# Kernel optimization log

Measured on AMD Instinct MI355X. Metric: run time of the kernel, lower is better.

## Reference

```python
import jax, jax.numpy as jnp
import numpy as np

N, E, H, L, G, C = 50000, 800000, 64, 4, 500, 10
BN_EPS = 1e-5


def setup_inputs() -> dict:
    key = jax.random.key(0)
    ks = jax.random.split(key, 24)
    x = jax.random.normal(ks[0], (N, H), dtype=jnp.float32)
    edge_index = jax.random.randint(ks[1], (2, E), 0, N, dtype=jnp.int64)
    batch = jnp.sort(jax.random.randint(ks[2], (N,), 0, G, dtype=jnp.int64))
    s = 1.0 / np.sqrt(H)
    # stacked per-layer GIN MLP params: Linear->BN->ReLU->Linear->BN->ReLU
    conv_W1 = jax.random.uniform(ks[3], (L, H, H), minval=-s, maxval=s, dtype=jnp.float32)
    conv_b1 = jax.random.uniform(ks[4], (L, H), minval=-s, maxval=s, dtype=jnp.float32)
    bn1_g = jax.random.uniform(ks[5], (L, H), minval=0.5, maxval=1.5, dtype=jnp.float32)
    bn1_b = jax.random.normal(ks[6], (L, H), dtype=jnp.float32) * 0.1
    bn1_m = jax.random.normal(ks[7], (L, H), dtype=jnp.float32) * 0.1
    bn1_v = jax.random.uniform(ks[8], (L, H), minval=0.5, maxval=1.5, dtype=jnp.float32)
    conv_W2 = jax.random.uniform(ks[9], (L, H, H), minval=-s, maxval=s, dtype=jnp.float32)
    conv_b2 = jax.random.uniform(ks[10], (L, H), minval=-s, maxval=s, dtype=jnp.float32)
    bn2_g = jax.random.uniform(ks[11], (L, H), minval=0.5, maxval=1.5, dtype=jnp.float32)
    bn2_b = jax.random.normal(ks[12], (L, H), dtype=jnp.float32) * 0.1
    bn2_m = jax.random.normal(ks[13], (L, H), dtype=jnp.float32) * 0.1
    bn2_v = jax.random.uniform(ks[14], (L, H), minval=0.5, maxval=1.5, dtype=jnp.float32)
    s1 = 1.0 / np.sqrt(L * H)
    lin1_W = jax.random.uniform(ks[15], (L * H, H), minval=-s1, maxval=s1, dtype=jnp.float32)
    lin1_b = jax.random.uniform(ks[16], (H,), minval=-s1, maxval=s1, dtype=jnp.float32)
    lin2_W = jax.random.uniform(ks[17], (H, C), minval=-s, maxval=s, dtype=jnp.float32)
    lin2_b = jax.random.uniform(ks[18], (C,), minval=-s, maxval=s, dtype=jnp.float32)
    return dict(x=x, edge_index=edge_index, batch=batch,
                conv_W1=conv_W1, conv_b1=conv_b1, bn1_g=bn1_g, bn1_b=bn1_b, bn1_m=bn1_m, bn1_v=bn1_v,
                conv_W2=conv_W2, conv_b2=conv_b2, bn2_g=bn2_g, bn2_b=bn2_b, bn2_m=bn2_m, bn2_v=bn2_v,
                lin1_W=lin1_W, lin1_b=lin1_b, lin2_W=lin2_W, lin2_b=lin2_b)


def _bn(h, g, b, m, v):
    # eval-mode BatchNorm1d with running stats
    return g * (h - m) * jax.lax.rsqrt(v + BN_EPS) + b


def reference(x, edge_index, batch,
              conv_W1, conv_b1, bn1_g, bn1_b, bn1_m, bn1_v,
              conv_W2, conv_b2, bn2_g, bn2_b, bn2_m, bn2_v,
              lin1_W, lin1_b, lin2_W, lin2_b):
    src, dst = edge_index[0], edge_index[1]

    def layer(h, p):
        W1, b1, g1, be1, m1, v1, W2, b2, g2, be2, m2, v2 = p
        # GIN aggregation (eps=0): h_i + sum_{j->i} h_j, scatter-add over edges
        agg = jax.ops.segment_sum(h[src], dst, num_segments=N)
        z = h + agg
        z = jax.nn.relu(_bn(z @ W1 + b1, g1, be1, m1, v1))
        z = jax.nn.relu(_bn(z @ W2 + b2, g2, be2, m2, v2))
        return z, z

    params = (conv_W1, conv_b1, bn1_g, bn1_b, bn1_m, bn1_v,
              conv_W2, conv_b2, bn2_g, bn2_b, bn2_m, bn2_v)
    _, xs = jax.lax.scan(layer, x, params)          # [L, N, H]
    xcat = jnp.transpose(xs, (1, 0, 2)).reshape(N, L * H)  # JK 'cat'
    pooled = jax.ops.segment_sum(xcat, batch, num_segments=G)  # sum readout [G, L*H]
    h = jax.nn.relu(pooled @ lin1_W + lin1_b)
    # dropout is identity in eval mode
    return h @ lin2_W + lin2_b  # [G, C]
```

## Files before the change

kernel.cpp:

```cpp
#include <hip/hip_runtime.h>

#define NN 50000
#define NE 800000
#define HH 64
#define LL 4
#define GG 500
#define CC 10
#define BN_EPS 1e-5f
#define SCB 200
#define NPART 6250
#define ECHUNK 2048
#define NCHUNK 391

typedef short bf16x8 __attribute__((ext_vector_type(8)));
typedef float f32x4  __attribute__((ext_vector_type(4)));

__device__ inline float bf2f(unsigned int u16) {
    union { unsigned int i; float f; } v; v.i = u16 << 16; return v.f;
}
__device__ inline unsigned short f2bf(float f) {
    union { float f; unsigned int i; } v; v.f = f;
    unsigned int u = v.i + 0x7fffu + ((v.i >> 16) & 1u);
    return (unsigned short)(u >> 16);
}
__device__ inline void addrow8(float* acc, uint4 u) {
    #pragma unroll
    for (int q = 0; q < 4; ++q) {
        unsigned int w = (&u.x)[q];
        union { unsigned int i; float f; } lo, hi;
        lo.i = w << 16; hi.i = w & 0xffff0000u;
        acc[2 * q]     += lo.f;
        acc[2 * q + 1] += hi.f;
    }
}

__global__ __launch_bounds__(256) void k_cast(const float* __restrict__ x, unsigned short* __restrict__ xb) {
    int i = blockIdx.x * 256 + threadIdx.x;
    if (i < NN * 16) {
        float4 v = ((const float4*)x)[i];
        uint2 p;
        p.x = (unsigned int)f2bf(v.x) | ((unsigned int)f2bf(v.y) << 16);
        p.y = (unsigned int)f2bf(v.z) | ((unsigned int)f2bf(v.w) << 16);
        ((uint2*)xb)[i] = p;
    }
}

__global__ __launch_bounds__(256) void k_prepw(const float* __restrict__ cW1,
                                               const float* __restrict__ cW2,
                                               unsigned short* __restrict__ fragW)
{
    int idx = blockIdx.x * 256 + threadIdx.x;
    if (idx >= LL * 2 * 4 * 2 * 64 * 8) return;
    int j    = idx & 7;
    int lane = (idx >> 3) & 63;
    int kh   = (idx >> 9) & 1;
    int ct   = (idx >> 10) & 3;
    int g    = (idx >> 12) & 1;
    int L    = idx >> 13;
    int k = kh * 32 + (lane >> 4) * 8 + j;
    int n = ct * 16 + (lane & 15);
    const float* W = (g == 0 ? cW1 : cW2) + (size_t)L * HH * HH;
    float w = W[k * HH + n];
    unsigned short hi = f2bf(w);
    unsigned short lo = f2bf(w - bf2f(hi));
    size_t fhi = ((size_t)L * 32 + ((g * 2 + 0) * 4 + ct) * 2 + kh) * 512 + lane * 8 + j;
    size_t flo = ((size_t)L * 32 + ((g * 2 + 1) * 4 + ct) * 2 + kh) * 512 + lane * 8 + j;
    fragW[fhi] = hi;
    fragW[flo] = lo;
}

__global__ __launch_bounds__(256) void k_hist8(const int* __restrict__ dst, int* __restrict__ deg) {
    int part  = blockIdx.x & 7;
    int chunk = blockIdx.x >> 3;
    int lo = part * NPART, hi = lo + NPART;
    int base = chunk * ECHUNK + threadIdx.x;
    #pragma unroll
    for (int i = 0; i < 8; ++i) {
        int e = base + i * 256;
        if (e < NE) {
            int d = dst[e];
            if (d >= lo && d < hi) atomicAdd(&deg[d], 1);
        }
    }
}

__global__ __launch_bounds__(256) void k_scan1(const int* __restrict__ deg, int* __restrict__ incl,
                                               int* __restrict__ bsum) {
    int t = threadIdx.x;
    int idx = blockIdx.x * 256 + t;
    __shared__ int s[256];
    int v = (idx < NN) ? deg[idx] : 0;
    s[t] = v;
    __syncthreads();
    for (int off = 1; off < 256; off <<= 1) {
        int u = (t >= off) ? s[t - off] : 0;
        __syncthreads();
        if (t >= off) s[t] += u;
        __syncthreads();
    }
    if (idx < NN) incl[idx] = s[t];
    if (t == 255) bsum[blockIdx.x] = s[255];
}

__global__ __launch_bounds__(256) void k_scan2(const int* __restrict__ bsum, int* __restrict__ boff,
                                               int* __restrict__ row_ptr) {
    int t = threadIdx.x;
    __shared__ int s[256];
    int v = (t < SCB) ? bsum[t] : 0;
    s[t] = v;
    __syncthreads();
    for (int off = 1; off < 256; off <<= 1) {
        int u = (t >= off) ? s[t - off] : 0;
        __syncthreads();
        if (t >= off) s[t] += u;
        __syncthreads();
    }
    if (t < SCB) boff[t] = s[t] - v;
    if (t == 255) row_ptr[NN] = s[255];
}

__global__ __launch_bounds__(256) void k_scan3(const int* __restrict__ deg, const int* __restrict__ incl,
                                               const int* __restrict__ boff, int* __restrict__ row_ptr) {
    int idx = blockIdx.x * 256 + threadIdx.x;
    if (idx < NN) row_ptr[idx] = incl[idx] - deg[idx] + boff[blockIdx.x];
}

__global__ __launch_bounds__(256) void k_scatter8(const int* __restrict__ src, const int* __restrict__ dst,
                                                  const int* __restrict__ row_ptr, int* __restrict__ cursor,
                                                  int* __restrict__ col) {
    int part  = blockIdx.x & 7;
    int chunk = blockIdx.x >> 3;
    int lo = part * NPART, hi = lo + NPART;
    int base = chunk * ECHUNK + threadIdx.x;
    #pragma unroll
    for (int i = 0; i < 8; ++i) {
        int e = base + i * 256;
        if (e < NE) {
            int d = dst[e];
            if (d >= lo && d < hi) {
                int pos = atomicAdd(&cursor[d], 1);
                col[row_ptr[d] + pos] = src[e];
            }
        }
    }
}

__global__ __launch_bounds__(256) void k_agg(
    const unsigned short* __restrict__ hb, unsigned short* __restrict__ aggb,
    const int* __restrict__ row_ptr, const int* __restrict__ col)
{
    int tid  = threadIdx.x;
    int lane = tid & 63;
    int wave = tid >> 6;
    int gl   = lane & 7;
    int grp  = lane >> 3;
    int n = blockIdx.x * 32 + wave * 8 + grp;
    if (n >= NN) return;

    const uint4* hv = (const uint4*)hb;
    float acc[8]  = {0.f, 0.f, 0.f, 0.f, 0.f, 0.f, 0.f, 0.f};
    float acc2[8] = {0.f, 0.f, 0.f, 0.f, 0.f, 0.f, 0.f, 0.f};
    addrow8(acc, hv[(size_t)n * 8 + gl]);

    int j = row_ptr[n], fin = row_ptr[n + 1];
    for (; j + 4 <= fin; j += 4) {
        int s0 = col[j], s1 = col[j + 1], s2 = col[j + 2], s3 = col[j + 3];
        uint4 u0 = hv[(size_t)s0 * 8 + gl];
        uint4 u1 = hv[(size_t)s1 * 8 + gl];
        uint4 u2 = hv[(size_t)s2 * 8 + gl];
        uint4 u3 = hv[(size_t)s3 * 8 + gl];
        addrow8(acc, u0);  addrow8(acc2, u1);
        addrow8(acc, u2);  addrow8(acc2, u3);
    }
    for (; j < fin; ++j)
        addrow8(acc, hv[(size_t)col[j] * 8 + gl]);

    #pragma unroll
    for (int q = 0; q < 8; ++q) acc[q] += acc2[q];

    uint4 o;
    o.x = (unsigned int)f2bf(acc[0]) | ((unsigned int)f2bf(acc[1]) << 16);
    o.y = (unsigned int)f2bf(acc[2]) | ((unsigned int)f2bf(acc[3]) << 16);
    o.z = (unsigned int)f2bf(acc[4]) | ((unsigned int)f2bf(acc[5]) << 16);
    o.w = (unsigned int)f2bf(acc[6]) | ((unsigned int)f2bf(acc[7]) << 16);
    ((uint4*)(aggb + (size_t)n * HH))[gl] = o;
}

#define MT 128
#define SAB 80
#define SOF 68

__global__ __launch_bounds__(256) void k_mlp2(
    const unsigned short* __restrict__ agg, unsigned short* __restrict__ h_out,
    const int* __restrict__ batch, float* __restrict__ pooled, int layer,
    const unsigned short* __restrict__ fragW,
    const float* __restrict__ lb1, const float* __restrict__ g1,
    const float* __restrict__ bb1, const float* __restrict__ m1, const float* __restrict__ v1,
    const float* __restrict__ lb2, const float* __restrict__ g2,
    const float* __restrict__ bb2, const float* __restrict__ m2, const float* __restrict__ v2)
{
    __shared__ unsigned short sHi[128 * SAB];
    __shared__ unsigned short sLo[128 * SAB];
    __shared__ float sOut[128 * SOF];
    __shared__ float red[256];

    int tid  = threadIdx.x;
    int lane = tid & 63;
    int wave = tid >> 6;
    int l15 = lane & 15, l4 = lane >> 4;
    int base = blockIdx.x * MT;
    int wrow = wave * 32;

    float sc1v[4], sh1v[4], sc2v[4], sh2v[4];
    #pragma unroll
    for (int ct = 0; ct < 4; ++ct) {
        int c = ct * 16 + l15;
        float s1 = g1[c] * rsqrtf(v1[c] + BN_EPS);
        sc1v[ct] = s1; sh1v[ct] = (lb1[c] - m1[c]) * s1 + bb1[c];
        float s2 = g2[c] * rsqrtf(v2[c] + BN_EPS);
        sc2v[ct] = s2; sh2v[ct] = (lb2[c] - m2[c]) * s2 + bb2[c];
    }

    for (int i = tid; i < 128 * 8; i += 256) {
        int r = i >> 3, q = i & 7;
        int gr = base + r;
        uint4 u = (gr < NN) ? ((const uint4*)(agg + (size_t)gr * HH))[q] : make_uint4(0, 0, 0, 0);
        *(uint4*)&sHi[r * SAB + q * 8] = u;
    }
    __syncthreads();

    const bf16x8* fwv = (const bf16x8*)fragW + ((size_t)layer * 32) * 64;

    bf16x8 a0[2][2];
    #pragma unroll
    for (int rt = 0; rt < 2; ++rt)
        #pragma unroll
        for (int kh = 0; kh < 2; ++kh)
            a0[rt][kh] = *(const bf16x8*)&sHi[(wrow + rt * 16 + l15) * SAB + kh * 32 + l4 * 8];

    f32x4 acc[2][4];
    #pragma unroll
    for (int rt = 0; rt < 2; ++rt)
        #pragma unroll
        for (int ct = 0; ct < 4; ++ct) {
            f32x4 c = {0.f, 0.f, 0.f, 0.f};
            #pragma unroll
            for (int kh = 0; kh < 2; ++kh) {
                c = __builtin_amdgcn_mfma_f32_16x16x32_bf16(a0[rt][kh], fwv[((0 * 4 + ct) * 2 + kh) * 64 + lane], c, 0, 0, 0);
                c = __builtin_amdgcn_mfma_f32_16x16x32_bf16(a0[rt][kh], fwv[((1 * 4 + ct) * 2 + kh) * 64 + lane], c, 0, 0, 0);
            }
            acc[rt][ct] = c;
        }
    __syncthreads();

    #pragma unroll
    for (int rt = 0; rt < 2; ++rt)
        #pragma unroll
        for (int ct = 0; ct < 4; ++ct)
            #pragma unroll
            for (int rg = 0; rg < 4; ++rg) {
                int r = wrow + rt * 16 + l4 * 4 + rg;
                float z = fmaxf(fmaf(acc[rt][ct][rg], sc1v[ct], sh1v[ct]), 0.f);
                unsigned short hi = f2bf(z);
                sHi[r * SAB + ct * 16 + l15] = hi;
                sLo[r * SAB + ct * 16 + l15] = f2bf(z - bf2f(hi));
            }
    __syncthreads();

    bf16x8 ah[2][2], al[2][2];
    #pragma unroll
    for (int rt = 0; rt < 2; ++rt)
        #pragma unroll
        for (int kh = 0; kh < 2; ++kh) {
            int off = (wrow + rt * 16 + l15) * SAB + kh * 32 + l4 * 8;
            ah[rt][kh] = *(const bf16x8*)&sHi[off];
            al[rt][kh] = *(const bf16x8*)&sLo[off];
        }
    #pragma unroll
    for (int rt = 0; rt < 2; ++rt)
        #pragma unroll
        for (int ct = 0; ct < 4; ++ct) {
            f32x4 c = {0.f, 0.f, 0.f, 0.f};
            #pragma unroll
            for (int kh = 0; kh < 2; ++kh) {
                bf16x8 bh = fwv[((2 * 4 + ct) * 2 + kh) * 64 + lane];
                bf16x8 bl = fwv[((3 * 4 + ct) * 2 + kh) * 64 + lane];
                c = __builtin_amdgcn_mfma_f32_16x16x32_bf16(ah[rt][kh], bh, c, 0, 0, 0);
                c = __builtin_amdgcn_mfma_f32_16x16x32_bf16(al[rt][kh], bh, c, 0, 0, 0);
                c = __builtin_amdgcn_mfma_f32_16x16x32_bf16(ah[rt][kh], bl, c, 0, 0, 0);
            }
            #pragma unroll
            for (int rg = 0; rg < 4; ++rg) {
                int r = wrow + rt * 16 + l4 * 4 + rg;
                float z = fmaxf(fmaf(c[rg], sc2v[ct], sh2v[ct]), 0.f);
                sOut[r * SOF + ct * 16 + l15] = z;
            }
        }
    __syncthreads();

    for (int i = tid; i < 128 * 8; i += 256) {
        int r = i >> 3, q = i & 7;
        int gr = base + r;
        if (gr < NN) {
            const float* sp = &sOut[r * SOF + q * 8];
            uint4 o;
            o.x = (unsigned int)f2bf(sp[0]) | ((unsigned int)f2bf(sp[1]) << 16);
            o.y = (unsigned int)f2bf(sp[2]) | ((unsigned int)f2bf(sp[3]) << 16);
            o.z = (unsigned int)f2bf(sp[4]) | ((unsigned int)f2bf(sp[5]) << 16);
            o.w = (unsigned int)f2bf(sp[6]) | ((unsigned int)f2bf(sp[7]) << 16);
            ((uint4*)(h_out + (size_t)gr * HH))[q] = o;
        }
    }

    int thi = base + MT; if (thi > NN) thi = NN;
    int gfirst = batch[base];
    int glast  = batch[thi - 1];
    int c = tid & 63;
    int q = tid >> 6;
    for (int g = gfirst; g <= glast; ++g) {
        int lo = base, hb = thi;
        while (lo < hb) { int mid = (lo + hb) >> 1; if (batch[mid] < g) lo = mid + 1; else hb = mid; }
        int lo_g = lo;
        hb = thi;
        while (lo < hb) { int mid = (lo + hb) >> 1; if (batch[mid] < g + 1) lo = mid + 1; else hb = mid; }
        int hi_g = lo;
        float a = 0.f;
        for (int r = lo_g + q; r < hi_g; r += 4) a += sOut[(r - base) * SOF + c];
        red[tid] = a;
        __syncthreads();
        if (tid < 64)
            atomicAdd(&pooled[(size_t)g * (LL * HH) + layer * HH + c],
                      red[c] + red[64 + c] + red[128 + c] + red[192 + c]);
        __syncthreads();
    }
}

__global__ __launch_bounds__(64) void k_mlp(const float* __restrict__ pooled,
                                            const float* __restrict__ w1, const float* __restrict__ b1,
                                            const float* __restrict__ w2, const float* __restrict__ b2,
                                            float* __restrict__ out)
{
    int g = blockIdx.x, c = threadIdx.x;
    __shared__ float hh[64];
    float acc = b1[c];
    const float* p = pooled + g * (LL * HH);
    #pragma unroll 8
    for (int k = 0; k < LL * HH; ++k) acc = fmaf(p[k], w1[k * HH + c], acc);
    hh[c] = fmaxf(acc, 0.f);
    __syncthreads();
    if (c < CC) {
        float o = b2[c];
        #pragma unroll
        for (int k = 0; k < HH; ++k) o = fmaf(hh[k], w2[k * CC + c], o);
        out[g * CC + c] = o;
    }
}

extern "C" void kernel_launch(void* const* d_in, const int* in_sizes, int n_in,
                              void* d_out, int out_size, void* d_ws, size_t ws_size,
                              hipStream_t stream) {
    const float* x    = (const float*)d_in[0];
    const int*   ei   = (const int*)d_in[1];
    const int*   bat  = (const int*)d_in[2];
    const float* cW1  = (const float*)d_in[3];
    const float* cb1  = (const float*)d_in[4];
    const float* g1   = (const float*)d_in[5];
    const float* bb1  = (const float*)d_in[6];
    const float* m1   = (const float*)d_in[7];
    const float* v1   = (const float*)d_in[8];
    const float* cW2  = (const float*)d_in[9];
    const float* cb2  = (const float*)d_in[10];
    const float* g2   = (const float*)d_in[11];
    const float* bb2  = (const float*)d_in[12];
    const float* m2   = (const float*)d_in[13];
    const float* v2   = (const float*)d_in[14];
    const float* l1W  = (const float*)d_in[15];
    const float* l1b  = (const float*)d_in[16];
    const float* l2W  = (const float*)d_in[17];
    const float* l2b  = (const float*)d_in[18];

    const int* srcp = ei;
    const int* dstp = ei + NE;

    char* ws = (char*)d_ws;
    size_t off = 0;
    auto alloc = [&](size_t bytes) -> char* {
        char* p = ws + off;
        off += (bytes + 255) & ~size_t(255);
        return p;
    };
    unsigned short* xb    = (unsigned short*)alloc((size_t)NN * HH * 2);
    unsigned short* hb0   = (unsigned short*)alloc((size_t)NN * HH * 2);
    unsigned short* hb1   = (unsigned short*)alloc((size_t)NN * HH * 2);
    unsigned short* aggb  = (unsigned short*)alloc((size_t)NN * HH * 2);
    unsigned short* fragW = (unsigned short*)alloc((size_t)LL * 32 * 512 * 2);
    float* pooled  = (float*)alloc((size_t)GG * LL * HH * sizeof(float));
    int*   row_ptr = (int*)alloc((size_t)(NN + 1) * sizeof(int));
    int*   deg     = (int*)alloc((size_t)NN * sizeof(int));
    int*   incl    = (int*)alloc((size_t)NN * sizeof(int));
    int*   cursor  = (int*)alloc((size_t)NN * sizeof(int));
    int*   colx    = (int*)alloc((size_t)NE * sizeof(int));
    int*   bsum    = (int*)alloc(256 * sizeof(int));
    int*   boff    = (int*)alloc(256 * sizeof(int));

    hipMemsetAsync(deg, 0, (size_t)NN * sizeof(int), stream);
    hipMemsetAsync(cursor, 0, (size_t)NN * sizeof(int), stream);
    hipMemsetAsync(pooled, 0, (size_t)GG * LL * HH * sizeof(float), stream);

    k_hist8<<<8 * NCHUNK, 256, 0, stream>>>(dstp, deg);
    k_cast<<<NN * 16 / 256, 256, 0, stream>>>(x, xb);
    k_prepw<<<128, 256, 0, stream>>>(cW1, cW2, fragW);
    k_scan1<<<SCB, 256, 0, stream>>>(deg, incl, bsum);
    k_scan2<<<1, 256, 0, stream>>>(bsum, boff, row_ptr);
    k_scan3<<<SCB, 256, 0, stream>>>(deg, incl, boff, row_ptr);
    k_scatter8<<<8 * NCHUNK, 256, 0, stream>>>(srcp, dstp, row_ptr, cursor, colx);

    const unsigned short* hin = xb;
    unsigned short* bufs[2] = { hb0, hb1 };
    const int AGG_BLK = (NN + 31) / 32;
    const int MLP_BLK = (NN + MT - 1) / MT;
    for (int l = 0; l < LL; ++l) {
        unsigned short* hout = bufs[l & 1];
        k_agg<<<AGG_BLK, 256, 0, stream>>>(hin, aggb, row_ptr, colx);
        k_mlp2<<<MLP_BLK, 256, 0, stream>>>(aggb, hout, bat, pooled, l, fragW,
            cb1 + l * HH, g1 + l * HH, bb1 + l * HH, m1 + l * HH, v1 + l * HH,
            cb2 + l * HH, g2 + l * HH, bb2 + l * HH, m2 + l * HH, v2 + l * HH);
        hin = hout;
    }

    k_mlp<<<GG, 64, 0, stream>>>(pooled, l1W, l1b, l2W, l2b, (float*)d_out);
}
```

Before: 315.1 us.

## Merge prep kernels and scan stages, coalesce memsets, unroll aggregation by eight

Fuses the cast and weight-prep kernels into one launch, and folds the single-block scan into the final scan pass so that each block recomputes the block-offset prefix itself. The three memsets are replaced by one, made possible by placing the zeroed buffers next to each other in the workspace. The aggregation loop gains an 8-wide unrolled gather to keep more loads in flight. These reduce launch count and per-launch overhead, at the cost of redundant prefix work in every scan block and higher register pressure in k_agg.

```diff
diff --git a/kernel.cpp b/kernel.cpp
--- a/kernel.cpp
+++ b/kernel.cpp
@@ -11,6 +11,7 @@
 #define NPART 6250
 #define ECHUNK 2048
 #define NCHUNK 391
+#define CASTB 3125
 
 typedef short bf16x8 __attribute__((ext_vector_type(8)));
 typedef float f32x4  __attribute__((ext_vector_type(4)));
@@ -34,22 +35,22 @@
     }
 }
 
-__global__ __launch_bounds__(256) void k_cast(const float* __restrict__ x, unsigned short* __restrict__ xb) {
-    int i = blockIdx.x * 256 + threadIdx.x;
-    if (i < NN * 16) {
-        float4 v = ((const float4*)x)[i];
-        uint2 p;
-        p.x = (unsigned int)f2bf(v.x) | ((unsigned int)f2bf(v.y) << 16);
-        p.y = (unsigned int)f2bf(v.z) | ((unsigned int)f2bf(v.w) << 16);
-        ((uint2*)xb)[i] = p;
-    }
-}
-
-__global__ __launch_bounds__(256) void k_prepw(const float* __restrict__ cW1,
-                                               const float* __restrict__ cW2,
-                                               unsigned short* __restrict__ fragW)
+__global__ __launch_bounds__(256) void k_prep(const float* __restrict__ x, unsigned short* __restrict__ xb,
+                                              const float* __restrict__ cW1, const float* __restrict__ cW2,
+                                              unsigned short* __restrict__ fragW)
 {
-    int idx = blockIdx.x * 256 + threadIdx.x;
+    if (blockIdx.x < CASTB) {
+        int i = blockIdx.x * 256 + threadIdx.x;
+        if (i < NN * 16) {
+            float4 v = ((const float4*)x)[i];
+            uint2 p;
+            p.x = (unsigned int)f2bf(v.x) | ((unsigned int)f2bf(v.y) << 16);
+            p.y = (unsigned int)f2bf(v.z) | ((unsigned int)f2bf(v.w) << 16);
+            ((uint2*)xb)[i] = p;
+        }
+        return;
+    }
+    int idx = (blockIdx.x - CASTB) * 256 + threadIdx.x;
     if (idx >= LL * 2 * 4 * 2 * 64 * 8) return;
     int j    = idx & 7;
     int lane = (idx >> 3) & 63;
@@ -102,8 +103,8 @@
     if (t == 255) bsum[blockIdx.x] = s[255];
 }
 
-__global__ __launch_bounds__(256) void k_scan2(const int* __restrict__ bsum, int* __restrict__ boff,
-                                               int* __restrict__ row_ptr) {
+__global__ __launch_bounds__(256) void k_scan3f(const int* __restrict__ deg, const int* __restrict__ incl,
+                                                const int* __restrict__ bsum, int* __restrict__ row_ptr) {
     int t = threadIdx.x;
     __shared__ int s[256];
     int v = (t < SCB) ? bsum[t] : 0;
@@ -115,14 +116,10 @@
         if (t >= off) s[t] += u;
         __syncthreads();
     }
-    if (t < SCB) boff[t] = s[t] - v;
-    if (t == 255) row_ptr[NN] = s[255];
-}
-
-__global__ __launch_bounds__(256) void k_scan3(const int* __restrict__ deg, const int* __restrict__ incl,
-                                               const int* __restrict__ boff, int* __restrict__ row_ptr) {
-    int idx = blockIdx.x * 256 + threadIdx.x;
-    if (idx < NN) row_ptr[idx] = incl[idx] - deg[idx] + boff[blockIdx.x];
+    int boff_b = (blockIdx.x == 0) ? 0 : s[blockIdx.x - 1];
+    if (blockIdx.x == 0 && t == 0) row_ptr[NN] = s[SCB - 1];
+    int idx = blockIdx.x * 256 + t;
+    if (idx < NN) row_ptr[idx] = incl[idx] - deg[idx] + boff_b;
 }
 
 __global__ __launch_bounds__(256) void k_scatter8(const int* __restrict__ src, const int* __restrict__ dst,
@@ -163,6 +160,22 @@
     addrow8(acc, hv[(size_t)n * 8 + gl]);
 
     int j = row_ptr[n], fin = row_ptr[n + 1];
+    for (; j + 8 <= fin; j += 8) {
+        int s0 = col[j],     s1 = col[j + 1], s2 = col[j + 2], s3 = col[j + 3];
+        int s4 = col[j + 4], s5 = col[j + 5], s6 = col[j + 6], s7 = col[j + 7];
+        uint4 u0 = hv[(size_t)s0 * 8 + gl];
+        uint4 u1 = hv[(size_t)s1 * 8 + gl];
+        uint4 u2 = hv[(size_t)s2 * 8 + gl];
+        uint4 u3 = hv[(size_t)s3 * 8 + gl];
+        uint4 u4 = hv[(size_t)s4 * 8 + gl];
+        uint4 u5 = hv[(size_t)s5 * 8 + gl];
+        uint4 u6 = hv[(size_t)s6 * 8 + gl];
+        uint4 u7 = hv[(size_t)s7 * 8 + gl];
+        addrow8(acc, u0);  addrow8(acc2, u1);
+        addrow8(acc, u2);  addrow8(acc2, u3);
+        addrow8(acc, u4);  addrow8(acc2, u5);
+        addrow8(acc, u6);  addrow8(acc2, u7);
+    }
     for (; j + 4 <= fin; j += 4) {
         int s0 = col[j], s1 = col[j + 1], s2 = col[j + 2], s3 = col[j + 3];
         uint4 u0 = hv[(size_t)s0 * 8 + gl];
@@ -394,25 +407,21 @@
     unsigned short* hb1   = (unsigned short*)alloc((size_t)NN * HH * 2);
     unsigned short* aggb  = (unsigned short*)alloc((size_t)NN * HH * 2);
     unsigned short* fragW = (unsigned short*)alloc((size_t)LL * 32 * 512 * 2);
+    int*   deg     = (int*)alloc((size_t)NN * sizeof(int));
+    int*   cursor  = (int*)alloc((size_t)NN * sizeof(int));
     float* pooled  = (float*)alloc((size_t)GG * LL * HH * sizeof(float));
+    size_t zspan   = (size_t)((char*)(pooled + (size_t)GG * LL * HH) - (char*)deg);
     int*   row_ptr = (int*)alloc((size_t)(NN + 1) * sizeof(int));
-    int*   deg     = (int*)alloc((size_t)NN * sizeof(int));
     int*   incl    = (int*)alloc((size_t)NN * sizeof(int));
-    int*   cursor  = (int*)alloc((size_t)NN * sizeof(int));
     int*   colx    = (int*)alloc((size_t)NE * sizeof(int));
     int*   bsum    = (int*)alloc(256 * sizeof(int));
-    int*   boff    = (int*)alloc(256 * sizeof(int));
-
-    hipMemsetAsync(deg, 0, (size_t)NN * sizeof(int), stream);
-    hipMemsetAsync(cursor, 0, (size_t)NN * sizeof(int), stream);
-    hipMemsetAsync(pooled, 0, (size_t)GG * LL * HH * sizeof(float), stream);
+
+    hipMemsetAsync(deg, 0, zspan, stream);
 
     k_hist8<<<8 * NCHUNK, 256, 0, stream>>>(dstp, deg);
-    k_cast<<<NN * 16 / 256, 256, 0, stream>>>(x, xb);
-    k_prepw<<<128, 256, 0, stream>>>(cW1, cW2, fragW);
+    k_prep<<<CASTB + 128, 256, 0, stream>>>(x, xb, cW1, cW2, fragW);
     k_scan1<<<SCB, 256, 0, stream>>>(deg, incl, bsum);
-    k_scan2<<<1, 256, 0, stream>>>(bsum, boff, row_ptr);
-    k_scan3<<<SCB, 256, 0, stream>>>(deg, incl, boff, row_ptr);
+    k_scan3f<<<SCB, 256, 0, stream>>>(deg, incl, bsum, row_ptr);
     k_scatter8<<<8 * NCHUNK, 256, 0, stream>>>(srcp, dstp, row_ptr, cursor, colx);
 
     const unsigned short* hin = xb;
```

After: 314.5 us. About the same (-0.2%).
